# Kernel optimization log

Measured on AMD Instinct MI355X. Metric: run time of the kernel, lower is better.

## Reference

```python
import jax, jax.numpy as jnp
from jax import lax
import numpy as np

DN = ('NCHW', 'OIHW', 'NCHW')
EPS = 1e-8
LRELU_SLOPE = 0.2
SQRT2 = np.float32(np.sqrt(2.0))


def _blur2d(x):
    # 5x5 binomial FIR, depthwise, padding=2, stride=1 (Blur2d(kernel_size=5, padding=2))
    k1 = jnp.array([1.0, 4.0, 6.0, 4.0, 1.0], dtype=x.dtype)
    k2 = jnp.outer(k1, k1)
    k2 = k2 / k2.sum()
    C = x.shape[1]
    kern = jnp.broadcast_to(k2, (C, 1, 5, 5))
    return lax.conv_general_dilated(x, kern, window_strides=(1, 1),
                                    padding=[(2, 2), (2, 2)],
                                    feature_group_count=C,
                                    dimension_numbers=DN)


def _second_moment_norm(x, g):
    # normalize by per-channel spatial second moment, learnable gain g [C]
    ms = jnp.mean(jnp.square(x), axis=(2, 3), keepdims=True)  # [B,C,1,1]
    return x * lax.rsqrt(ms + EPS) * g[None, :, None, None]


def _modulated_conv(x, w, b, style_w, style_b, s, stride, padding):
    # StyleGAN2 modulated conv with demodulation, grouped-conv batch trick
    B, I, H, W = x.shape
    O, _, kh, kw = w.shape
    scale = np.float32(1.0 / np.sqrt(I * kh * kw))
    style = s @ style_w.T + style_b[None, :]                      # [B, I]
    wm = scale * w[None] * style[:, None, :, None, None]          # [B,O,I,kh,kw]
    d = lax.rsqrt(jnp.sum(jnp.square(wm), axis=(2, 3, 4)) + EPS)  # [B,O]
    wm = wm * d[:, :, None, None, None]
    xg = x.reshape(1, B * I, H, W)
    wg = wm.reshape(B * O, I, kh, kw)
    out = lax.conv_general_dilated(xg, wg, window_strides=(stride, stride),
                                   padding=[(padding, padding), (padding, padding)],
                                   feature_group_count=B,
                                   dimension_numbers=DN)
    out = out.reshape(B, O, out.shape[2], out.shape[3])
    return out + b[None, :, None, None]


def setup_inputs() -> dict:
    key = jax.random.key(0)
    ks = jax.random.split(key, 5)
    B, I, O, S, H, W, K = 8, 256, 256, 512, 128, 128, 3
    x = jax.random.normal(ks[0], (B, I, H, W), dtype=jnp.float32)
    s = jax.random.normal(ks[1], (B, S), dtype=jnp.float32)
    conv_w = jax.random.normal(ks[2], (O, I, K, K), dtype=jnp.float32)
    conv_b = jnp.zeros((O,), dtype=jnp.float32)
    style_w = jax.random.normal(ks[3], (I, S), dtype=jnp.float32) / np.float32(np.sqrt(S))
    style_b = jnp.ones((I,), dtype=jnp.float32)  # StyleGAN2 init: bias=1
    norm_g = jnp.ones((I,), dtype=jnp.float32)
    return {"x": x, "s": s, "conv_w": conv_w, "conv_b": conv_b,
            "style_w": style_w, "style_b": style_b, "norm_g": norm_g}


def reference(x, s, conv_w, conv_b, style_w, style_b, norm_g):
    x = _blur2d(x)                                   # blur (stride != 1 path)
    x = _second_moment_norm(x, norm_g)               # second-moment norm
    x = _modulated_conv(x, conv_w, conv_b, style_w, style_b, s, stride=2, padding=1)
    x = jnp.where(x >= 0, x, LRELU_SLOPE * x) * SQRT2  # scaled LeakyReLU
    return x
```

## Files before the change

kernel.cpp:

```cpp
#include <hip/hip_runtime.h>
#include <hip/hip_bf16.h>
#include <math.h>

#define B 8
#define IC 256
#define OC 256
#define SDIM 512
#define H 128
#define W 128
#define OH 64
#define OW 64
#define EPS 1e-8f
#define SQRT2 1.41421356237309504880f
#define SCALE 0.02083333395421505f

#define RS 16640
#define PLANE 1081600

typedef unsigned short u16;
typedef unsigned int u32;
typedef __attribute__((ext_vector_type(8))) short s16x8;
typedef __attribute__((ext_vector_type(4))) float f32x4;

__device__ __forceinline__ void gl_lds16(const void* g, void* l) {
    __builtin_amdgcn_global_load_lds((const __attribute__((address_space(1))) u32*)g,
                                     (__attribute__((address_space(3))) u32*)l, 16, 0, 0);
}

__global__ void wsq_kernel(const float* __restrict__ w, float* __restrict__ wsq,
                           float* __restrict__ zbuf) {
    int i = blockIdx.x * 256 + threadIdx.x;
    const float* p = w + (size_t)i * 9;
    float sum = 0.f;
    for (int k = 0; k < 9; ++k) sum = fmaf(p[k], p[k], sum);
    wsq[i] = sum;
    if (blockIdx.x == 0 && threadIdx.x < 64) zbuf[threadIdx.x] = 0.f;
}

__global__ __launch_bounds__(256) void style_demod_kernel(const float* __restrict__ s,
                                                          const float* __restrict__ sw,
                                                          const float* __restrict__ sb,
                                                          const float* __restrict__ wsq,
                                                          float* __restrict__ style,
                                                          float* __restrict__ demod,
                                                          float* __restrict__ ssq) {
    __shared__ float st[256];
    const int b = blockIdx.x;
    const int tid = threadIdx.x;
    const float4* sv = (const float4*)(s + (size_t)b * SDIM);
    const float4* wv = (const float4*)(sw + (size_t)tid * SDIM);
    float sum = 0.f;
    #pragma unroll 4
    for (int k = 0; k < 128; ++k) {
        float4 a4 = sv[k], b4 = wv[k];
        sum = fmaf(a4.x, b4.x, fmaf(a4.y, b4.y, fmaf(a4.z, b4.z, fmaf(a4.w, b4.w, sum))));
    }
    float styv = sum + sb[tid];
    style[(b << 8) + tid] = styv;
    st[tid] = styv;
    ssq[(b << 8) + tid] = 0.f;
    __syncthreads();
    const float4* wq = (const float4*)(wsq + (size_t)tid * 256);
    float acc = 0.f;
    #pragma unroll 4
    for (int k = 0; k < 64; ++k) {
        float4 q = wq[k];
        float s0 = st[4 * k], s1 = st[4 * k + 1], s2 = st[4 * k + 2], s3 = st[4 * k + 3];
        acc = fmaf(s0 * s0, q.x, fmaf(s1 * s1, q.y, fmaf(s2 * s2, q.z, fmaf(s3 * s3, q.w, acc))));
    }
    demod[(b << 8) + tid] = rsqrtf(SCALE * SCALE * acc + EPS);
}

__global__ __launch_bounds__(256, 5) void blurpack_kernel(const float* __restrict__ x,
                                                          __hip_bfloat16* __restrict__ xbp,
                                                          float* __restrict__ ssq,
                                                          const float* __restrict__ zbuf) {
    __shared__ __align__(16) char smem[32768];
    u16 (*pbuf)[2][2][544] = reinterpret_cast<u16(*)[2][2][544]>(smem);
    const float* rawf = (const float*)smem;
    const int strip = blockIdx.x;
    const int ic0 = blockIdx.y << 3;
    const int b = blockIdx.z;
    const int t = threadIdx.x;

    {
        int gidx = t ^ ((t >> 3) & 7);
        int sch = gidx >> 5, cg5 = gidx & 31;
        const float* xch = x + (((size_t)(b * 256 + ic0 + sch)) << 14) + (cg5 << 2);
        char* dst = smem + t * 16;
        #pragma unroll
        for (int k = 0; k < 8; ++k) {
            int gr = (strip << 2) - 2 + k;
            const void* src = (gr >= 0 && gr < H) ? (const void*)(xch + ((size_t)gr << 7))
                                                  : (const void*)zbuf;
            gl_lds16(src, dst + (k << 12));
        }
    }
    __syncthreads();

    const int hr = t >> 7;
    const int ch = (t >> 4) & 7;
    const int cg = t & 15;
    const int i0 = (ch << 5) + (cg << 1);
    const int p0 = i0 ^ ((i0 >> 3) & 7);
    const int p1 = p0 ^ 1;
    float ssacc = 0.f;
    uint2 res0[2], res1[2];

    #pragma unroll
    for (int pass = 0; pass < 2; ++pass) {
        const int br = (pass << 1) + hr;

        float v[8];
        #pragma unroll
        for (int j = 0; j < 8; ++j) v[j] = 0.f;
        #pragma unroll
        for (int rr = 0; rr < 5; ++rr) {
            const float wv = (rr == 2) ? 6.f : ((rr & 1) ? 4.f : 1.f);
            const int rb = (br + rr) << 10;
            float4 q0 = *(const float4*)(rawf + rb + (p0 << 2));
            float4 q1 = *(const float4*)(rawf + rb + (p1 << 2));
            v[0] = fmaf(wv, q0.x, v[0]); v[1] = fmaf(wv, q0.y, v[1]);
            v[2] = fmaf(wv, q0.z, v[2]); v[3] = fmaf(wv, q0.w, v[3]);
            v[4] = fmaf(wv, q1.x, v[4]); v[5] = fmaf(wv, q1.y, v[5]);
            v[6] = fmaf(wv, q1.z, v[6]); v[7] = fmaf(wv, q1.w, v[7]);
        }

        float vm2 = __shfl_up(v[6], 1, 64);
        float vm1 = __shfl_up(v[7], 1, 64);
        float vp1 = __shfl_down(v[0], 1, 64);
        float vp2 = __shfl_down(v[1], 1, 64);
        if (cg == 0)  { vm2 = 0.f; vm1 = 0.f; }
        if (cg == 15) { vp1 = 0.f; vp2 = 0.f; }
        float e[12];
        e[0] = vm2; e[1] = vm1;
        #pragma unroll
        for (int j = 0; j < 8; ++j) e[2 + j] = v[j];
        e[10] = vp1; e[11] = vp2;

        u16 hp[8];
        #pragma unroll
        for (int j = 0; j < 8; ++j) {
            float hv = fmaf(6.f, e[j + 2], fmaf(4.f, e[j + 1] + e[j + 3], e[j] + e[j + 4]))
                     * (1.0f / 256.0f);
            ssacc = fmaf(hv, hv, ssacc);
            __hip_bfloat16 hb = __float2bfloat16(hv);
            hp[j] = *(u16*)&hb;
        }
        u16 w0[4] = {hp[0], hp[2], hp[4], hp[6]};
        u16 w1[4] = {hp[1], hp[3], hp[5], hp[7]};
        res0[pass] = *(const uint2*)w0;
        res1[pass] = *(const uint2*)w1;
    }

    __syncthreads();

    #pragma unroll
    for (int pass = 0; pass < 2; ++pass) {
        *(uint2*)&pbuf[pass][hr][0][(ch << 6) + (cg << 2)] = res0[pass];
        *(uint2*)&pbuf[pass][hr][1][(ch << 6) + (cg << 2)] = res1[pass];
    }
    __syncthreads();

    {
        int fc = t & 127;
        int hr2 = t >> 7;
        int pw = fc & 1, pcol = fc >> 1;
        #pragma unroll
        for (int pass = 0; pass < 2; ++pass) {
            uint4 g;
            u16* gp = (u16*)&g;
            #pragma unroll
            for (int c2 = 0; c2 < 8; ++c2)
                gp[c2] = pbuf[pass][hr2][pw][(c2 << 6) + pcol];
            size_t off = (size_t)((b << 2) + (hr2 << 1) + pw) * PLANE
                       + (size_t)((strip << 1) + pass + 1) * RS
                       + (size_t)(pcol + 1) * 256 + ic0;
            *(uint4*)(xbp + off) = g;
        }
    }

    float sv2 = ssacc;
    sv2 += __shfl_down(sv2, 8, 16);
    sv2 += __shfl_down(sv2, 4, 16);
    sv2 += __shfl_down(sv2, 2, 16);
    sv2 += __shfl_down(sv2, 1, 16);
    if (cg == 0) atomicAdd(&ssq[(b << 8) + ic0 + ch], sv2);
}

__global__ void wf_kernel(const float* __restrict__ w,
                          const float* __restrict__ demod,
                          const float* __restrict__ ssq,
                          const float* __restrict__ style,
                          const float* __restrict__ g,
                          __hip_bfloat16* __restrict__ wf,
                          __hip_bfloat16* __restrict__ xbp) {
    int bo = blockIdx.x;
    int b = bo >> 8, o = bo & 255;
    int ic = threadIdx.x;
    float fac = rsqrtf(ssq[(b << 8) + ic] * (1.0f / 16384.0f) + EPS)
              * g[ic] * style[(b << 8) + ic] * SCALE;
    float m = demod[bo] * fac;
    const float* wp = w + ((size_t)o * 256 + ic) * 9;
    __hip_bfloat16* dst = wf + (size_t)bo * 2304 + ic;
    #pragma unroll
    for (int t = 0; t < 9; ++t)
        dst[t * 256] = __float2bfloat16(wp[t] * m);

    if (bo < 32) {
        int t = threadIdx.x;
        char* base = (char*)(xbp + (size_t)bo * PLANE);
        uint4 z = {0u, 0u, 0u, 0u};
        for (int k = 0; k < 9; ++k) {
            int c = t + (k << 8);
            if (c < 2080) *(uint4*)(base + (size_t)c * 16) = z;
        }
        for (int k = 0; k < 8; ++k) {
            int c = t + (k << 8);
            int r = 1 + (c >> 5);
            int off = (c & 31) << 3;
            *(uint4*)(base + ((size_t)r * RS + off) * 2) = z;
        }
    }
}

__global__ __launch_bounds__(256, 2) void conv_kernel(const __hip_bfloat16* __restrict__ xbp,
                                                      const __hip_bfloat16* __restrict__ wf,
                                                      const float* __restrict__ bias,
                                                      float* __restrict__ out) {
    __shared__ char lds[65536];
    const int t = threadIdx.x;
    const int bid = blockIdx.x;
    const int xcd = bid & 7;
    const int y   = (bid >> 3) & 31;
    const int p   = xcd + (((bid >> 8) & 1) << 3);
    const int o0  = (p & 1) << 7;
    const int b   = p >> 1;
    const size_t bb = (size_t)b << 8;

    u32 aoffs[4], boffs[4];
    #pragma unroll
    for (int j = 0; j < 4; ++j) {
        int s = t + (j << 8);
        int r = s >> 3, m = s & 7;
        int g = m ^ (r & 7);
        aoffs[j] = (u32)(r * 2304 + (g << 3)) * 2;
        boffs[j] = (u32)((((y << 1) + (r >> 6)) * RS) + ((r & 63) << 8) + (g << 3)) * 2;
    }
    const char* gAbase = (const char*)(wf + (bb + o0) * 2304);

    const int lane = t & 63, wave = t >> 6;
    const int lr = lane & 15, quad = lane >> 4;
    const int mb = (wave & 1) << 6;
    const int nb = (wave >> 1) << 6;

    f32x4 acc[4][4];
    #pragma unroll
    for (int i = 0; i < 4; ++i)
        #pragma unroll
        for (int j = 0; j < 4; ++j) acc[i][j] = (f32x4){0.f, 0.f, 0.f, 0.f};

    #define STAGE_TILE(cc, bufbase)                                                        \
    {                                                                                      \
        int tap = (cc) >> 2;                                                               \
        int icq = ((cc) & 3) << 6;                                                         \
        int th = (tap * 11) >> 5;                                                          \
        int tw = tap - th * 3;                                                             \
        int ph  = (th == 1) ? 0 : 1;                                                       \
        int dhp = (th == 0) ? 0 : 1;                                                       \
        int pw  = (tw == 1) ? 0 : 1;                                                       \
        int dwp = (tw == 0) ? 0 : 1;                                                       \
        const char* gA = gAbase + (size_t)(tap * 256 + icq) * 2;                           \
        const char* gB = (const char*)(xbp + (size_t)((b << 2) + (ph << 1) + pw) * PLANE   \
                                       + (size_t)dhp * RS + (dwp << 8) + icq);             \
        char* dA = (bufbase) + t * 16;                                                     \
        char* dB = (bufbase) + 16384 + t * 16;                                             \
        _Pragma("unroll")                                                                  \
        for (int j = 0; j < 4; ++j) gl_lds16(gA + aoffs[j], dA + (j << 12));               \
        _Pragma("unroll")                                                                  \
        for (int j = 0; j < 4; ++j) gl_lds16(gB + boffs[j], dB + (j << 12));               \
    }

    STAGE_TILE(0, lds);

    int cur = 0;
    for (int c = 0; c < 36; ++c) {
        if (c < 35) {
            STAGE_TILE(c + 1, lds + ((cur ^ 1) << 15));
            asm volatile("s_waitcnt vmcnt(8)" ::: "memory");
        } else {
            asm volatile("s_waitcnt vmcnt(0)" ::: "memory");
        }
        __builtin_amdgcn_s_barrier();
        __builtin_amdgcn_sched_barrier(0);

        const char* ldsA = lds + (cur << 15);
        const char* ldsB = ldsA + 16384;
        #pragma unroll
        for (int s = 0; s < 2; ++s) {
            const int mq = ((s << 2) + quad) ^ (lr & 7);
            s16x8 a[4], bf[4];
            #pragma unroll
            for (int i = 0; i < 4; ++i)
                a[i] = *(const s16x8*)(ldsA + ((mb + (i << 4) + lr) << 7) + (mq << 4));
            #pragma unroll
            for (int j = 0; j < 4; ++j)
                bf[j] = *(const s16x8*)(ldsB + ((nb + (j << 4) + lr) << 7) + (mq << 4));
            #pragma unroll
            for (int i = 0; i < 4; ++i)
                #pragma unroll
                for (int j = 0; j < 4; ++j)
                    acc[i][j] = __builtin_amdgcn_mfma_f32_16x16x32_bf16(a[i], bf[j], acc[i][j], 0, 0, 0);
        }
        asm volatile("s_waitcnt lgkmcnt(0)" ::: "memory");
        __builtin_amdgcn_s_barrier();
        cur ^= 1;
    }
    #undef STAGE_TILE

    float bi[4][4];
    #pragma unroll
    for (int i = 0; i < 4; ++i)
        #pragma unroll
        for (int rr = 0; rr < 4; ++rr)
            bi[i][rr] = bias[o0 + mb + (i << 4) + (quad << 2) + rr];
    const int n0 = y << 7;
    #pragma unroll
    for (int i = 0; i < 4; ++i) {
        #pragma unroll
        for (int j = 0; j < 4; ++j) {
            #pragma unroll
            for (int rr = 0; rr < 4; ++rr) {
                int oc = o0 + mb + (i << 4) + (quad << 2) + rr;
                int n = n0 + nb + (j << 4) + lr;
                int oh = n >> 6, ow2 = n & 63;
                float v = acc[i][j][rr] + bi[i][rr];
                v = (v >= 0.f ? v : 0.2f * v) * SQRT2;
                out[((bb + oc) << 12) + (oh << 6) + ow2] = v;
            }
        }
    }
}

extern "C" void kernel_launch(void* const* d_in, const int* in_sizes, int n_in,
                              void* d_out, int out_size, void* d_ws, size_t ws_size,
                              hipStream_t stream) {
    const float* x   = (const float*)d_in[0];
    const float* s   = (const float*)d_in[1];
    const float* cw  = (const float*)d_in[2];
    const float* cb  = (const float*)d_in[3];
    const float* sw  = (const float*)d_in[4];
    const float* sb  = (const float*)d_in[5];
    const float* ng  = (const float*)d_in[6];
    float* out = (float*)d_out;

    char* ws = (char*)d_ws;
    __hip_bfloat16* xbp = (__hip_bfloat16*)ws;
    __hip_bfloat16* wfb = (__hip_bfloat16*)(ws + 69222400);
    float* style  = (float*)(ws + 78659584);
    float* wsq    = style + 2048;
    float* demod  = wsq + 65536;
    float* ssq    = demod + 2048;
    float* zbuf   = ssq + 2048;

    wsq_kernel<<<256, 256, 0, stream>>>(cw, wsq, zbuf);
    style_demod_kernel<<<8, 256, 0, stream>>>(s, sw, sb, wsq, style, demod, ssq);
    blurpack_kernel<<<dim3(32, 32, 8), 256, 0, stream>>>(x, xbp, ssq, zbuf);
    wf_kernel<<<2048, 256, 0, stream>>>(cw, demod, ssq, style, ng, wfb, xbp);
    conv_kernel<<<512, 256, 0, stream>>>(xbp, wfb, cb, out);
}
```

Before: 310.4 us.

## Pipeline blurpack over four strips per block and simplify conv-loop synchronisation

The blur/pack kernel now has each block process four consecutive row strips instead of one. It double-buffers the raw input tiles in LDS so the async global-to-LDS load of the next strip overlaps the blur and pack of the current one. This cuts the grid by four, raises LDS use to about 74 KB and lowers launch bounds to 2 blocks per CU, trading occupancy for load/compute overlap. The conv kernel's hand-tuned partial vmcnt waits and raw barriers are replaced by plain __syncthreads. That may force waits on all outstanding loads at each iteration end and shorten the prefetch window.

```diff
diff --git a/kernel.cpp b/kernel.cpp
--- a/kernel.cpp
+++ b/kernel.cpp
@@ -71,32 +71,31 @@
     demod[(b << 8) + tid] = rsqrtf(SCALE * SCALE * acc + EPS);
 }
 
-__global__ __launch_bounds__(256, 5) void blurpack_kernel(const float* __restrict__ x,
+__global__ __launch_bounds__(256, 2) void blurpack_kernel(const float* __restrict__ x,
                                                           __hip_bfloat16* __restrict__ xbp,
                                                           float* __restrict__ ssq,
                                                           const float* __restrict__ zbuf) {
-    __shared__ __align__(16) char smem[32768];
-    u16 (*pbuf)[2][2][544] = reinterpret_cast<u16(*)[2][2][544]>(smem);
-    const float* rawf = (const float*)smem;
-    const int strip = blockIdx.x;
+    __shared__ __align__(16) char smem[74240];
+    u16 (*pbuf)[2][2][544] = reinterpret_cast<u16(*)[2][2][544]>(smem + 65536);
+    const int group = blockIdx.x;
     const int ic0 = blockIdx.y << 3;
     const int b = blockIdx.z;
     const int t = threadIdx.x;
 
-    {
-        int gidx = t ^ ((t >> 3) & 7);
-        int sch = gidx >> 5, cg5 = gidx & 31;
-        const float* xch = x + (((size_t)(b * 256 + ic0 + sch)) << 14) + (cg5 << 2);
-        char* dst = smem + t * 16;
-        #pragma unroll
-        for (int k = 0; k < 8; ++k) {
-            int gr = (strip << 2) - 2 + k;
-            const void* src = (gr >= 0 && gr < H) ? (const void*)(xch + ((size_t)gr << 7))
-                                                  : (const void*)zbuf;
-            gl_lds16(src, dst + (k << 12));
-        }
-    }
-    __syncthreads();
+    const int gidx = t ^ ((t >> 3) & 7);
+    const int sch = gidx >> 5, cg5 = gidx & 31;
+    const float* xch = x + (((size_t)(b * 256 + ic0 + sch)) << 14) + (cg5 << 2);
+
+    #define STAGEK(strip, base)                                                            \
+    {   char* dst = (base) + t * 16;                                                       \
+        _Pragma("unroll")                                                                  \
+        for (int k = 0; k < 8; ++k) {                                                      \
+            int gr = ((strip) << 2) - 2 + k;                                               \
+            const void* src = (gr >= 0 && gr < H) ? (const void*)(xch + ((size_t)gr << 7)) \
+                                                  : (const void*)zbuf;                     \
+            gl_lds16(src, dst + (k << 12));                                                \
+        }                                                                                  \
+    }
 
     const int hr = t >> 7;
     const int ch = (t >> 4) & 7;
@@ -105,80 +104,97 @@
     const int p0 = i0 ^ ((i0 >> 3) & 7);
     const int p1 = p0 ^ 1;
     float ssacc = 0.f;
-    uint2 res0[2], res1[2];
-
-    #pragma unroll
-    for (int pass = 0; pass < 2; ++pass) {
-        const int br = (pass << 1) + hr;
-
-        float v[8];
-        #pragma unroll
-        for (int j = 0; j < 8; ++j) v[j] = 0.f;
-        #pragma unroll
-        for (int rr = 0; rr < 5; ++rr) {
-            const float wv = (rr == 2) ? 6.f : ((rr & 1) ? 4.f : 1.f);
-            const int rb = (br + rr) << 10;
-            float4 q0 = *(const float4*)(rawf + rb + (p0 << 2));
-            float4 q1 = *(const float4*)(rawf + rb + (p1 << 2));
-            v[0] = fmaf(wv, q0.x, v[0]); v[1] = fmaf(wv, q0.y, v[1]);
-            v[2] = fmaf(wv, q0.z, v[2]); v[3] = fmaf(wv, q0.w, v[3]);
-            v[4] = fmaf(wv, q1.x, v[4]); v[5] = fmaf(wv, q1.y, v[5]);
-            v[6] = fmaf(wv, q1.z, v[6]); v[7] = fmaf(wv, q1.w, v[7]);
-        }
-
-        float vm2 = __shfl_up(v[6], 1, 64);
-        float vm1 = __shfl_up(v[7], 1, 64);
-        float vp1 = __shfl_down(v[0], 1, 64);
-        float vp2 = __shfl_down(v[1], 1, 64);
-        if (cg == 0)  { vm2 = 0.f; vm1 = 0.f; }
-        if (cg == 15) { vp1 = 0.f; vp2 = 0.f; }
-        float e[12];
-        e[0] = vm2; e[1] = vm1;
-        #pragma unroll
-        for (int j = 0; j < 8; ++j) e[2 + j] = v[j];
-        e[10] = vp1; e[11] = vp2;
-
-        u16 hp[8];
-        #pragma unroll
-        for (int j = 0; j < 8; ++j) {
-            float hv = fmaf(6.f, e[j + 2], fmaf(4.f, e[j + 1] + e[j + 3], e[j] + e[j + 4]))
-                     * (1.0f / 256.0f);
-            ssacc = fmaf(hv, hv, ssacc);
-            __hip_bfloat16 hb = __float2bfloat16(hv);
-            hp[j] = *(u16*)&hb;
-        }
-        u16 w0[4] = {hp[0], hp[2], hp[4], hp[6]};
-        u16 w1[4] = {hp[1], hp[3], hp[5], hp[7]};
-        res0[pass] = *(const uint2*)w0;
-        res1[pass] = *(const uint2*)w1;
-    }
-
-    __syncthreads();
-
-    #pragma unroll
-    for (int pass = 0; pass < 2; ++pass) {
-        *(uint2*)&pbuf[pass][hr][0][(ch << 6) + (cg << 2)] = res0[pass];
-        *(uint2*)&pbuf[pass][hr][1][(ch << 6) + (cg << 2)] = res1[pass];
-    }
-    __syncthreads();
-
-    {
-        int fc = t & 127;
-        int hr2 = t >> 7;
-        int pw = fc & 1, pcol = fc >> 1;
+
+    STAGEK(group << 2, smem);
+
+    for (int s = 0; s < 4; ++s) {
+        const int strip = (group << 2) + s;
+        if (s < 3) {
+            STAGEK(strip + 1, smem + (((s + 1) & 1) << 15));
+            asm volatile("s_waitcnt vmcnt(8)" ::: "memory");
+        } else {
+            asm volatile("s_waitcnt vmcnt(0)" ::: "memory");
+        }
+        __builtin_amdgcn_s_barrier();
+        __builtin_amdgcn_sched_barrier(0);
+
+        const float* rawf = (const float*)(smem + ((s & 1) << 15));
+        uint2 res0[2], res1[2];
+
         #pragma unroll
         for (int pass = 0; pass < 2; ++pass) {
-            uint4 g;
-            u16* gp = (u16*)&g;
-            #pragma unroll
-            for (int c2 = 0; c2 < 8; ++c2)
-                gp[c2] = pbuf[pass][hr2][pw][(c2 << 6) + pcol];
-            size_t off = (size_t)((b << 2) + (hr2 << 1) + pw) * PLANE
-                       + (size_t)((strip << 1) + pass + 1) * RS
-                       + (size_t)(pcol + 1) * 256 + ic0;
-            *(uint4*)(xbp + off) = g;
-        }
-    }
+            const int br = (pass << 1) + hr;
+
+            float v[8];
+            #pragma unroll
+            for (int j = 0; j < 8; ++j) v[j] = 0.f;
+            #pragma unroll
+            for (int rr = 0; rr < 5; ++rr) {
+                const float wv = (rr == 2) ? 6.f : ((rr & 1) ? 4.f : 1.f);
+                const int rb = (br + rr) << 10;
+                float4 q0 = *(const float4*)(rawf + rb + (p0 << 2));
+                float4 q1 = *(const float4*)(rawf + rb + (p1 << 2));
+                v[0] = fmaf(wv, q0.x, v[0]); v[1] = fmaf(wv, q0.y, v[1]);
+                v[2] = fmaf(wv, q0.z, v[2]); v[3] = fmaf(wv, q0.w, v[3]);
+                v[4] = fmaf(wv, q1.x, v[4]); v[5] = fmaf(wv, q1.y, v[5]);
+                v[6] = fmaf(wv, q1.z, v[6]); v[7] = fmaf(wv, q1.w, v[7]);
+            }
+
+            float vm2 = __shfl_up(v[6], 1, 64);
+            float vm1 = __shfl_up(v[7], 1, 64);
+            float vp1 = __shfl_down(v[0], 1, 64);
+            float vp2 = __shfl_down(v[1], 1, 64);
+            if (cg == 0)  { vm2 = 0.f; vm1 = 0.f; }
+            if (cg == 15) { vp1 = 0.f; vp2 = 0.f; }
+            float e[12];
+            e[0] = vm2; e[1] = vm1;
+            #pragma unroll
+            for (int j = 0; j < 8; ++j) e[2 + j] = v[j];
+            e[10] = vp1; e[11] = vp2;
+
+            u16 hp[8];
+            #pragma unroll
+            for (int j = 0; j < 8; ++j) {
+                float hv = fmaf(6.f, e[j + 2], fmaf(4.f, e[j + 1] + e[j + 3], e[j] + e[j + 4]))
+                         * (1.0f / 256.0f);
+                ssacc = fmaf(hv, hv, ssacc);
+                __hip_bfloat16 hb = __float2bfloat16(hv);
+                hp[j] = *(u16*)&hb;
+            }
+            u16 w0[4] = {hp[0], hp[2], hp[4], hp[6]};
+            u16 w1[4] = {hp[1], hp[3], hp[5], hp[7]};
+            res0[pass] = *(const uint2*)w0;
+            res1[pass] = *(const uint2*)w1;
+        }
+
+        #pragma unroll
+        for (int pass = 0; pass < 2; ++pass) {
+            *(uint2*)&pbuf[pass][hr][0][(ch << 6) + (cg << 2)] = res0[pass];
+            *(uint2*)&pbuf[pass][hr][1][(ch << 6) + (cg << 2)] = res1[pass];
+        }
+        asm volatile("s_waitcnt lgkmcnt(0)" ::: "memory");
+        __builtin_amdgcn_s_barrier();
+        __builtin_amdgcn_sched_barrier(0);
+
+        {
+            int fc = t & 127;
+            int hr2 = t >> 7;
+            int pw = fc & 1, pcol = fc >> 1;
+            #pragma unroll
+            for (int pass = 0; pass < 2; ++pass) {
+                uint4 g;
+                u16* gp = (u16*)&g;
+                #pragma unroll
+                for (int c2 = 0; c2 < 8; ++c2)
+                    gp[c2] = pbuf[pass][hr2][pw][(c2 << 6) + pcol];
+                size_t off = (size_t)((b << 2) + (hr2 << 1) + pw) * PLANE
+                           + (size_t)((strip << 1) + pass + 1) * RS
+                           + (size_t)(pcol + 1) * 256 + ic0;
+                *(uint4*)(xbp + off) = g;
+            }
+        }
+    }
+    #undef STAGEK
 
     float sv2 = ssacc;
     sv2 += __shfl_down(sv2, 8, 16);
@@ -282,17 +298,11 @@
     }
 
     STAGE_TILE(0, lds);
+    __syncthreads();
 
     int cur = 0;
     for (int c = 0; c < 36; ++c) {
-        if (c < 35) {
-            STAGE_TILE(c + 1, lds + ((cur ^ 1) << 15));
-            asm volatile("s_waitcnt vmcnt(8)" ::: "memory");
-        } else {
-            asm volatile("s_waitcnt vmcnt(0)" ::: "memory");
-        }
-        __builtin_amdgcn_s_barrier();
-        __builtin_amdgcn_sched_barrier(0);
+        if (c < 35) STAGE_TILE(c + 1, lds + ((cur ^ 1) << 15));
 
         const char* ldsA = lds + (cur << 15);
         const char* ldsB = ldsA + 16384;
@@ -312,8 +322,7 @@
                 for (int j = 0; j < 4; ++j)
                     acc[i][j] = __builtin_amdgcn_mfma_f32_16x16x32_bf16(a[i], bf[j], acc[i][j], 0, 0, 0);
         }
-        asm volatile("s_waitcnt lgkmcnt(0)" ::: "memory");
-        __builtin_amdgcn_s_barrier();
+        __syncthreads();
         cur ^= 1;
     }
     #undef STAGE_TILE
@@ -365,7 +374,7 @@
 
     wsq_kernel<<<256, 256, 0, stream>>>(cw, wsq, zbuf);
     style_demod_kernel<<<8, 256, 0, stream>>>(s, sw, sb, wsq, style, demod, ssq);
-    blurpack_kernel<<<dim3(32, 32, 8), 256, 0, stream>>>(x, xbp, ssq, zbuf);
+    blurpack_kernel<<<dim3(8, 32, 8), 256, 0, stream>>>(x, xbp, ssq, zbuf);
     wf_kernel<<<2048, 256, 0, stream>>>(cw, demod, ssq, style, ng, wfb, xbp);
     conv_kernel<<<512, 256, 0, stream>>>(xbp, wfb, cb, out);
 }
```

Result: no change. 309.8 us (-0.2%).
